# Kernel tuning notes

Measured on AMD Instinct MI355X. Metric: run time of the kernel, lower is better.

The kernel has to match this reference:

```python
import jax, jax.numpy as jnp
import numpy as np

N_NODES = 100000
IN_CH = 128
HID_CH = 128
N_EDGES = 1600000


def setup_inputs() -> dict:
    key = jax.random.key(0)
    ks = jax.random.split(key, 8)
    x = jax.random.normal(ks[0], (N_NODES, IN_CH), dtype=jnp.float32)
    edge_index = jax.random.randint(ks[1], (2, N_EDGES), 0, N_NODES, dtype=jnp.int64)
    s1 = 1.0 / np.sqrt(IN_CH)
    s2 = 1.0 / np.sqrt(HID_CH)
    # SAGEConv layer 1: lin_l (aggregated neighbors, has bias), lin_r (root)
    Wl1 = jax.random.uniform(ks[2], (IN_CH, HID_CH), jnp.float32, -s1, s1)
    Wr1 = jax.random.uniform(ks[3], (IN_CH, HID_CH), jnp.float32, -s1, s1)
    b1 = jnp.zeros((HID_CH,), jnp.float32)
    # SAGEConv layer 2
    Wl2 = jax.random.uniform(ks[4], (HID_CH, HID_CH), jnp.float32, -s2, s2)
    Wr2 = jax.random.uniform(ks[5], (HID_CH, HID_CH), jnp.float32, -s2, s2)
    b2 = jnp.zeros((HID_CH,), jnp.float32)
    return {"x": x, "edge_index": edge_index,
            "Wl1": Wl1, "Wr1": Wr1, "b1": b1,
            "Wl2": Wl2, "Wr2": Wr2, "b2": b2}


def _sage_conv(x, src, dst, inv_deg, Wl, Wr, b):
    # mean aggregation of source-node features into destination nodes
    agg = jax.ops.segment_sum(x[src], dst, num_segments=N_NODES)  # [N, d]
    mean = agg * inv_deg[:, None]
    # out = lin_l(mean_neighbors) + lin_r(x)
    return mean @ Wl + x @ Wr + b


def reference(x, edge_index, Wl1, Wr1, b1, Wl2, Wr2, b2):
    src = edge_index[0]
    dst = edge_index[1]
    deg = jax.ops.segment_sum(jnp.ones_like(dst, dtype=jnp.float32), dst,
                              num_segments=N_NODES)
    inv_deg = 1.0 / jnp.maximum(deg, 1.0)
    h = jax.nn.relu(_sage_conv(x, src, dst, inv_deg, Wl1, Wr1, b1))
    # F.dropout(p=0.2, training=False) is identity in eval mode
    h = jax.nn.relu(_sage_conv(h, src, dst, inv_deg, Wl2, Wr2, b2))
    return h
```

## Files before the change

### kernel.cpp

```cpp
#include <hip/hip_runtime.h>

#define NN 100000
#define NE 1600000
#define CH 128

#define PART 512
#define NP 196
#define PCAP 8704
#define EPB 4096
#define NB 391
#define SCAP 64
#define SLAB 3072

typedef __attribute__((ext_vector_type(8))) short bf16x8;
typedef __attribute__((ext_vector_type(4))) float f32x4;
typedef unsigned int uint;
typedef unsigned short ushort;

__device__ __forceinline__ ushort f2b(float f) {
    uint u = __builtin_bit_cast(uint, f);
    uint r = (u + 0x7fff + ((u >> 16) & 1)) >> 16;
    return (ushort)r;
}
__device__ __forceinline__ float blo(uint v) { return __builtin_bit_cast(float, v << 16); }
__device__ __forceinline__ float bhi(uint v) { return __builtin_bit_cast(float, v & 0xffff0000u); }

__device__ __forceinline__ void acc8(float* a, uint4 v) {
    a[0] += blo(v.x); a[1] += bhi(v.x);
    a[2] += blo(v.y); a[3] += bhi(v.y);
    a[4] += blo(v.z); a[5] += bhi(v.z);
    a[6] += blo(v.w); a[7] += bhi(v.w);
}


__global__ __launch_bounds__(1024) void k_bin(const int4* __restrict__ src4, const int4* __restrict__ dst4,
                                              uint* __restrict__ pcnt, uint* __restrict__ pairbuf) {
    __shared__ uint slots[NP * SCAP];
    __shared__ uint lcnt[NP];
    __shared__ uint lbase[NP];
    int tid = threadIdx.x;
    if (tid < NP) lcnt[tid] = 0;
    __syncthreads();
    int e4 = blockIdx.x * 1024 + tid;
    if (e4 < NE / 4) {
        int4 d4 = dst4[e4];
        int4 s4 = src4[e4];
        int dd[4] = {d4.x, d4.y, d4.z, d4.w};
        int ss[4] = {s4.x, s4.y, s4.z, s4.w};
        #pragma unroll
        for (int j = 0; j < 4; ++j) {
            int p = dd[j] >> 9;
            uint pair = ((uint)(dd[j] & 511) << 17) | (uint)ss[j];
            uint pos = atomicAdd(&lcnt[p], 1u);
            if (pos < SCAP) slots[p * SCAP + pos] = pair;
        }
    }
    __syncthreads();
    if (tid < NP) {
        uint c = lcnt[tid];
        c = c < SCAP ? c : SCAP;
        lcnt[tid] = c;
        lbase[tid] = atomicAdd(&pcnt[tid], c);
    }
    __syncthreads();
    for (int t = tid; t < NP * SCAP; t += 1024) {
        int p = t >> 6;
        uint s = (uint)(t & (SCAP - 1));
        if (s < lcnt[p]) {
            uint idx = lbase[p] + s;
            if (idx < PCAP) pairbuf[(size_t)p * PCAP + idx] = slots[t];
        }
    }
}


__global__ __launch_bounds__(512) void k_csr(const uint* __restrict__ pcnt, const uint* __restrict__ pairbuf,
                                             int* __restrict__ nbrG, uint* __restrict__ pack) {
    __shared__ uint pairs[PCAP];
    __shared__ uint cnt[PART];
    __shared__ uint rowptr[PART + 1];
    __shared__ uint tsum[PART];
    int tid = threadIdx.x;
    int p = blockIdx.x;
    uint tot = pcnt[p];
    tot = tot < PCAP ? tot : PCAP;
    for (uint i = tid; i < tot; i += 512) pairs[i] = pairbuf[(size_t)p * PCAP + i];
    cnt[tid] = 0;
    __syncthreads();
    for (uint i = tid; i < tot; i += 512) atomicAdd(&cnt[pairs[i] >> 17], 1u);
    __syncthreads();
    uint s = cnt[tid];
    tsum[tid] = s;
    __syncthreads();
    for (int off = 1; off < 512; off <<= 1) {
        uint t = (tid >= off) ? tsum[tid - off] : 0;
        __syncthreads();
        tsum[tid] += t;
        __syncthreads();
    }
    rowptr[tid] = tsum[tid] - s;
    if (tid == 511) rowptr[512] = tsum[511];
    __syncthreads();
    cnt[tid] = 0;
    __syncthreads();
    for (uint i = tid; i < tot; i += 512) {
        uint u = pairs[i];
        uint dl = u >> 17;
        uint pos = rowptr[dl] + atomicAdd(&cnt[dl], 1u);
        nbrG[(size_t)p * PCAP + pos] = (int)(u & 0x1FFFFu);
    }
    {
        int n = p * PART + tid;
        if (n < NN) {
            uint deg = rowptr[tid + 1] - rowptr[tid];
            pack[n] = ((uint)(p * PCAP) + rowptr[tid]) | (deg << 21);
        }
    }
}


__global__ __launch_bounds__(256) void k_castx(const float* __restrict__ x, ushort* __restrict__ xb) {
    int n = blockIdx.x * 256 + threadIdx.x;
    int p = blockIdx.y;
    if (n >= NN) return;
    const float4* sp = (const float4*)(x + (size_t)n * 128 + p * 16);
    uint4 o[2];
    ushort* op = (ushort*)o;
    #pragma unroll
    for (int q = 0; q < 4; ++q) {
        float4 v = sp[q];
        op[q * 4 + 0] = f2b(v.x);
        op[q * 4 + 1] = f2b(v.y);
        op[q * 4 + 2] = f2b(v.z);
        op[q * 4 + 3] = f2b(v.w);
    }
    uint4* dp = (uint4*)(xb + ((size_t)p * NN + n) * 16);
    dp[0] = o[0];
    dp[1] = o[1];
}

__global__ __launch_bounds__(256) void k_castw(const float* __restrict__ Wl1, const float* __restrict__ Wr1,
                                               const float* __restrict__ Wl2, const float* __restrict__ Wr2,
                                               ushort* __restrict__ BtK1, ushort* __restrict__ BtK2) {
    int i = blockIdx.x * 256 + threadIdx.x;
    const float* Wl = blockIdx.y ? Wl2 : Wl1;
    const float* Wr = blockIdx.y ? Wr2 : Wr1;
    ushort* BtK = blockIdx.y ? BtK2 : BtK1;
    int c = i & 31;
    int n = (i >> 5) & 127;
    int kt = i >> 12;
    int k = kt * 32 + c;
    float v = (k < 128) ? Wl[k * 128 + n] : Wr[(k - 128) * 128 + n];
    BtK[i] = f2b(v);
}


__global__ __launch_bounds__(256) void k_agg(const uint4* __restrict__ feat, const int* __restrict__ nbrG,
                                             const uint* __restrict__ pack, uint4* __restrict__ outb) {
    __shared__ int sl[SLAB];
    __shared__ int sh_s0, sh_cnt;
    int plane = blockIdx.x;
    int nb = blockIdx.y * 128;
    int tid = threadIdx.x;
    int n = nb + (tid >> 1);
    int h = tid & 1;
    if (tid == 0) {
        uint u0 = pack[nb];
        int last = nb + 127 < NN ? nb + 127 : NN - 1;
        uint u1 = pack[last];
        int s0 = (int)(u0 & 0x1FFFFFu);
        sh_s0 = s0;
        sh_cnt = (int)(u1 & 0x1FFFFFu) + (int)(u1 >> 21) - s0;
    }
    __syncthreads();
    int s0 = sh_s0, scnt = sh_cnt;
    bool staged = scnt <= SLAB;
    if (staged) {
        for (int i = tid; i < scnt; i += 256) sl[i] = nbrG[s0 + i];
    }
    __syncthreads();
    if (n >= NN) return;
    uint u = pack[n];
    int s = (int)(u & 0x1FFFFFu);
    int d = (int)(u >> 21);
    const uint4* fp = feat + (size_t)plane * (NN * 2) + h;
    float a[8] = {};
    if (staged) {
        const int* bp = sl + (s - s0);
        int i = 0;
        for (; i + 8 <= d; i += 8) {
            int c[8];
            uint4 v[8];
            #pragma unroll
            for (int j = 0; j < 8; ++j) c[j] = bp[i + j];
            #pragma unroll
            for (int j = 0; j < 8; ++j) v[j] = fp[(size_t)c[j] * 2];
            #pragma unroll
            for (int j = 0; j < 8; ++j) acc8(a, v[j]);
        }
        for (; i < d; ++i) acc8(a, fp[(size_t)bp[i] * 2]);
    } else {
        const int* bp = nbrG + s;
        int i = 0;
        for (; i + 4 <= d; i += 4) {
            int c0 = bp[i], c1 = bp[i + 1], c2 = bp[i + 2], c3 = bp[i + 3];
            uint4 v0 = fp[(size_t)c0 * 2];
            uint4 v1 = fp[(size_t)c1 * 2];
            uint4 v2 = fp[(size_t)c2 * 2];
            uint4 v3 = fp[(size_t)c3 * 2];
            acc8(a, v0);
            acc8(a, v1);
            acc8(a, v2);
            acc8(a, v3);
        }
        for (; i < d; ++i) acc8(a, fp[(size_t)bp[i] * 2]);
    }
    float id = 1.0f / fmaxf((float)d, 1.0f);
    uint4 r;
    r.x = (uint)f2b(a[0] * id) | ((uint)f2b(a[1] * id) << 16);
    r.y = (uint)f2b(a[2] * id) | ((uint)f2b(a[3] * id) << 16);
    r.z = (uint)f2b(a[4] * id) | ((uint)f2b(a[5] * id) << 16);
    r.w = (uint)f2b(a[6] * id) | ((uint)f2b(a[7] * id) << 16);
    outb[((size_t)plane * NN + n) * 2 + h] = r;
}


template <bool WB16>
__global__ __launch_bounds__(256) void k_gemm(const ushort* __restrict__ Am, const ushort* Ax,
                                              const ushort* __restrict__ BtK, const float* __restrict__ bias,
                                              void* outp, int M) {
    int lane = threadIdx.x & 63;
    int wave = threadIdx.x >> 6;
    int bm = blockIdx.x * 128 + wave * 32;
    int l16 = lane & 15;
    int lk8 = (lane >> 4) * 8;

    f32x4 acc[2][8] = {};
    #pragma unroll
    for (int kt = 0; kt < 8; ++kt) {
        const ushort* A = (kt < 4) ? Am : Ax;
        int kA = (kt & 3) * 32 + lk8;
        int p = kA >> 4, ko = kA & 15;
        bf16x8 af[2];
        #pragma unroll
        for (int mt = 0; mt < 2; ++mt) {
            int row = bm + mt * 16 + l16;
            row = row < M ? row : M - 1;
            af[mt] = *(const bf16x8*)(A + ((size_t)p * NN + row) * 16 + ko);
        }
        const ushort* Bk = BtK + (size_t)kt * 128 * 32;
        #pragma unroll
        for (int nt = 0; nt < 8; ++nt) {
            bf16x8 bfr = *(const bf16x8*)(Bk + (size_t)(nt * 16 + l16) * 32 + lk8);
            acc[0][nt] = __builtin_amdgcn_mfma_f32_16x16x32_bf16(af[0], bfr, acc[0][nt], 0, 0, 0);
            acc[1][nt] = __builtin_amdgcn_mfma_f32_16x16x32_bf16(af[1], bfr, acc[1][nt], 0, 0, 0);
        }
    }
    int mr0 = (lane >> 4) * 4;
    #pragma unroll
    for (int mt = 0; mt < 2; ++mt) {
        #pragma unroll
        for (int r = 0; r < 4; ++r) {
            int m = bm + mt * 16 + mr0 + r;
            if (m < M) {
                #pragma unroll
                for (int nt = 0; nt < 8; ++nt) {
                    float v = acc[mt][nt][r] + bias[nt * 16 + l16];
                    v = v > 0.f ? v : 0.f;
                    if (WB16) {
                        ((ushort*)outp)[((size_t)nt * NN + m) * 16 + l16] = f2b(v);
                    } else {
                        ((float*)outp)[(size_t)m * 128 + nt * 16 + l16] = v;
                    }
                }
            }
        }
    }
}


static inline size_t alignup(size_t x) { return (x + 255) & ~(size_t)255; }

extern "C" void kernel_launch(void* const* d_in, const int* in_sizes, int n_in,
                              void* d_out, int out_size, void* d_ws, size_t ws_size,
                              hipStream_t stream) {
    const float* x   = (const float*)d_in[0];
    const int* edge  = (const int*)d_in[1];
    const float* Wl1 = (const float*)d_in[2];
    const float* Wr1 = (const float*)d_in[3];
    const float* b1  = (const float*)d_in[4];
    const float* Wl2 = (const float*)d_in[5];
    const float* Wr2 = (const float*)d_in[6];
    const float* b2  = (const float*)d_in[7];
    float* out = (float*)d_out;

    const int* srcp = edge;
    const int* dstp = edge + NE;

    uint* pairbuf = (uint*)d_out;
    int* nbrG = (int*)d_out + (size_t)NP * PCAP;

    char* w = (char*)d_ws;
    uint* pcnt = (uint*)w;     w += alignup((size_t)NP * 4);
    uint* pack = (uint*)w;     w += alignup((size_t)NN * 4);
    ushort* xb = (ushort*)w;   w += alignup((size_t)NN * CH * 2);
    ushort* mb = (ushort*)w;   w += alignup((size_t)NN * CH * 2);
    ushort* BtK1 = (ushort*)w; w += alignup((size_t)128 * 256 * 2);
    ushort* BtK2 = (ushort*)w; w += alignup((size_t)128 * 256 * 2);

    hipMemsetAsync(pcnt, 0, (size_t)NP * 4, stream);

    k_bin<<<NB, 1024, 0, stream>>>((const int4*)srcp, (const int4*)dstp, pcnt, pairbuf);
    k_csr<<<NP, 512, 0, stream>>>(pcnt, pairbuf, nbrG, pack);

    k_castx<<<dim3((NN + 255) / 256, 8), 256, 0, stream>>>(x, xb);
    k_castw<<<dim3(128, 2), 256, 0, stream>>>(Wl1, Wr1, Wl2, Wr2, BtK1, BtK2);

    int gg = (NN + 127) / 128;
    dim3 ag(8, (NN + 127) / 128);
    k_agg<<<ag, 256, 0, stream>>>((const uint4*)xb, nbrG, pack, (uint4*)mb);
    k_gemm<true><<<gg, 256, 0, stream>>>(mb, xb, BtK1, b1, (void*)xb, NN);
    k_agg<<<ag, 256, 0, stream>>>((const uint4*)xb, nbrG, pack, (uint4*)mb);
    k_gemm<false><<<gg, 256, 0, stream>>>(mb, xb, BtK2, b2, (void*)out, NN);
}
```

Before: 358.0 us.

## Widen bf16 feature planes to 32 channels for 64-byte gathers

Changes the plane-major bf16 feature layout from 8 planes of 16 channels to 4 planes of 32 channels, so each gathered neighbor row segment is 64 bytes read by 4 lanes instead of 32 bytes by 2 lanes. The cast, aggregation and GEMM load/store indexing are updated to match, aggregation blocks now cover 64 nodes with a smaller LDS neighbor slab, and gather addresses use 32-bit offset arithmetic. The aim is fewer, larger random gathers per edge and cheaper address computation. In exchange there are half as many planes per node for locality, and a higher fraction of blocks may fall back to the unstaged path.

```diff
diff --git a/kernel.cpp b/kernel.cpp
--- a/kernel.cpp
+++ b/kernel.cpp
@@ -10,7 +10,7 @@
 #define EPB 4096
 #define NB 391
 #define SCAP 64
-#define SLAB 3072
+#define SLAB 1536
 
 typedef __attribute__((ext_vector_type(8))) short bf16x8;
 typedef __attribute__((ext_vector_type(4))) float f32x4;
@@ -123,20 +123,20 @@
     int n = blockIdx.x * 256 + threadIdx.x;
     int p = blockIdx.y;
     if (n >= NN) return;
-    const float4* sp = (const float4*)(x + (size_t)n * 128 + p * 16);
-    uint4 o[2];
+    const float4* sp = (const float4*)(x + (size_t)n * 128 + p * 32);
+    uint4 o[4];
     ushort* op = (ushort*)o;
     #pragma unroll
-    for (int q = 0; q < 4; ++q) {
+    for (int q = 0; q < 8; ++q) {
         float4 v = sp[q];
         op[q * 4 + 0] = f2b(v.x);
         op[q * 4 + 1] = f2b(v.y);
         op[q * 4 + 2] = f2b(v.z);
         op[q * 4 + 3] = f2b(v.w);
     }
-    uint4* dp = (uint4*)(xb + ((size_t)p * NN + n) * 16);
-    dp[0] = o[0];
-    dp[1] = o[1];
+    uint4* dp = (uint4*)(xb + ((size_t)p * NN + n) * 32);
+    #pragma unroll
+    for (int q = 0; q < 4; ++q) dp[q] = o[q];
 }
 
 __global__ __launch_bounds__(256) void k_castw(const float* __restrict__ Wl1, const float* __restrict__ Wr1,
@@ -160,13 +160,13 @@
     __shared__ int sl[SLAB];
     __shared__ int sh_s0, sh_cnt;
     int plane = blockIdx.x;
-    int nb = blockIdx.y * 128;
+    int nb = blockIdx.y * 64;
     int tid = threadIdx.x;
-    int n = nb + (tid >> 1);
-    int h = tid & 1;
+    int n = nb + (tid >> 2);
+    int h = tid & 3;
     if (tid == 0) {
         uint u0 = pack[nb];
-        int last = nb + 127 < NN ? nb + 127 : NN - 1;
+        int last = nb + 63 < NN ? nb + 63 : NN - 1;
         uint u1 = pack[last];
         int s0 = (int)(u0 & 0x1FFFFFu);
         sh_s0 = s0;
@@ -183,37 +183,41 @@
     uint u = pack[n];
     int s = (int)(u & 0x1FFFFFu);
     int d = (int)(u >> 21);
-    const uint4* fp = feat + (size_t)plane * (NN * 2) + h;
+    const char* fb = (const char*)feat + ((size_t)plane * NN) * 64;
+    uint hoff = (uint)h * 16;
     float a[8] = {};
     if (staged) {
         const int* bp = sl + (s - s0);
         int i = 0;
         for (; i + 8 <= d; i += 8) {
-            int c[8];
+            uint off[8];
             uint4 v[8];
             #pragma unroll
-            for (int j = 0; j < 8; ++j) c[j] = bp[i + j];
+            for (int j = 0; j < 8; ++j) off[j] = ((uint)bp[i + j] << 6) | hoff;
             #pragma unroll
-            for (int j = 0; j < 8; ++j) v[j] = fp[(size_t)c[j] * 2];
+            for (int j = 0; j < 8; ++j) v[j] = *(const uint4*)(fb + off[j]);
             #pragma unroll
             for (int j = 0; j < 8; ++j) acc8(a, v[j]);
         }
-        for (; i < d; ++i) acc8(a, fp[(size_t)bp[i] * 2]);
+        for (; i < d; ++i) acc8(a, *(const uint4*)(fb + (((uint)bp[i] << 6) | hoff)));
     } else {
         const int* bp = nbrG + s;
         int i = 0;
         for (; i + 4 <= d; i += 4) {
-            int c0 = bp[i], c1 = bp[i + 1], c2 = bp[i + 2], c3 = bp[i + 3];
-            uint4 v0 = fp[(size_t)c0 * 2];
-            uint4 v1 = fp[(size_t)c1 * 2];
-            uint4 v2 = fp[(size_t)c2 * 2];
-            uint4 v3 = fp[(size_t)c3 * 2];
+            uint o0 = ((uint)bp[i] << 6) | hoff;
+            uint o1 = ((uint)bp[i + 1] << 6) | hoff;
+            uint o2 = ((uint)bp[i + 2] << 6) | hoff;
+            uint o3 = ((uint)bp[i + 3] << 6) | hoff;
+            uint4 v0 = *(const uint4*)(fb + o0);
+            uint4 v1 = *(const uint4*)(fb + o1);
+            uint4 v2 = *(const uint4*)(fb + o2);
+            uint4 v3 = *(const uint4*)(fb + o3);
             acc8(a, v0);
             acc8(a, v1);
             acc8(a, v2);
             acc8(a, v3);
         }
-        for (; i < d; ++i) acc8(a, fp[(size_t)bp[i] * 2]);
+        for (; i < d; ++i) acc8(a, *(const uint4*)(fb + (((uint)bp[i] << 6) | hoff)));
     }
     float id = 1.0f / fmaxf((float)d, 1.0f);
     uint4 r;
@@ -221,7 +225,7 @@
     r.y = (uint)f2b(a[2] * id) | ((uint)f2b(a[3] * id) << 16);
     r.z = (uint)f2b(a[4] * id) | ((uint)f2b(a[5] * id) << 16);
     r.w = (uint)f2b(a[6] * id) | ((uint)f2b(a[7] * id) << 16);
-    outb[((size_t)plane * NN + n) * 2 + h] = r;
+    outb[((size_t)plane * NN + n) * 4 + h] = r;
 }
 
 
@@ -239,14 +243,13 @@
     #pragma unroll
     for (int kt = 0; kt < 8; ++kt) {
         const ushort* A = (kt < 4) ? Am : Ax;
-        int kA = (kt & 3) * 32 + lk8;
-        int p = kA >> 4, ko = kA & 15;
+        int p = kt & 3;
         bf16x8 af[2];
         #pragma unroll
         for (int mt = 0; mt < 2; ++mt) {
             int row = bm + mt * 16 + l16;
             row = row < M ? row : M - 1;
-            af[mt] = *(const bf16x8*)(A + ((size_t)p * NN + row) * 16 + ko);
+            af[mt] = *(const bf16x8*)(A + ((size_t)p * NN + row) * 32 + lk8);
         }
         const ushort* Bk = BtK + (size_t)kt * 128 * 32;
         #pragma unroll
@@ -268,7 +271,8 @@
                     float v = acc[mt][nt][r] + bias[nt * 16 + l16];
                     v = v > 0.f ? v : 0.f;
                     if (WB16) {
-                        ((ushort*)outp)[((size_t)nt * NN + m) * 16 + l16] = f2b(v);
+                        int ch = nt * 16 + l16;
+                        ((ushort*)outp)[((size_t)(ch >> 5) * NN + m) * 32 + (ch & 31)] = f2b(v);
                     } else {
                         ((float*)outp)[(size_t)m * 128 + nt * 16 + l16] = v;
                     }
@@ -313,11 +317,11 @@
     k_bin<<<NB, 1024, 0, stream>>>((const int4*)srcp, (const int4*)dstp, pcnt, pairbuf);
     k_csr<<<NP, 512, 0, stream>>>(pcnt, pairbuf, nbrG, pack);
 
-    k_castx<<<dim3((NN + 255) / 256, 8), 256, 0, stream>>>(x, xb);
+    k_castx<<<dim3((NN + 255) / 256, 4), 256, 0, stream>>>(x, xb);
     k_castw<<<dim3(128, 2), 256, 0, stream>>>(Wl1, Wr1, Wl2, Wr2, BtK1, BtK2);
 
     int gg = (NN + 127) / 128;
-    dim3 ag(8, (NN + 127) / 128);
+    dim3 ag(4, (NN + 63) / 64);
     k_agg<<<ag, 256, 0, stream>>>((const uint4*)xb, nbrG, pack, (uint4*)mb);
     k_gemm<true><<<gg, 256, 0, stream>>>(mb, xb, BtK1, b1, (void*)xb, NN);
     k_agg<<<ag, 256, 0, stream>>>((const uint4*)xb, nbrG, pack, (uint4*)mb);
```

New measurement: 336.7 us. 1.06x faster.
